# Optimization experiments

Hardware: AMD Instinct MI355X
Metric: run time of the kernel (lower is better)

The kernel has to match this reference:

```python
import jax, jax.numpy as jnp
import numpy as np

B, N, M, D = 256, 256, 256, 4
BIG = 1e10  # stand-in for +inf that keeps grads of unselected branches finite


def chamfer_split(target, reco, in_pid, out_pid):
    # masks of 'real' (non-zero pid) particles
    mask_x = in_pid != 0          # [B, N]
    mask_y = out_pid != 0         # [B, M]
    nx = jnp.sum(mask_x, axis=-1)  # [B] actual counts
    ny = jnp.sum(mask_y, axis=-1)
    n_in = jnp.maximum(1, nx).astype(target.dtype)   # max(1, n_in_part)
    n_out = jnp.maximum(1, ny).astype(target.dtype)  # max(1, n_out_part)

    # pairwise euclidean distances [B, N, M]
    diff = target[:, :, None, :] - reco[:, None, :, :]   # [B, N, M, D]
    dist = jnp.sqrt(jnp.sum(diff * diff, axis=-1))       # [B, N, M]

    # masked dual-axis mins (invalid entries pushed to BIG)
    min_xy = jnp.min(jnp.where(mask_y[:, None, :], dist, BIG), axis=-1)  # [B, N]
    min_yx = jnp.min(jnp.where(mask_x[:, :, None], dist, BIG), axis=-2)  # [B, M]
    sum_xy = jnp.sum(jnp.where(mask_x, min_xy, 0.0), axis=-1)  # [B]
    sum_yx = jnp.sum(jnp.where(mask_y, min_yx, 0.0), axis=-1)  # [B]

    normal = 0.5 * (sum_xy / n_out + sum_yx / n_in)  # [B]

    # edge cases: no reco non-zero particles -> sum||x_nz|| / max(1,nx);
    # no target non-zero particles -> sum over empty set = 0
    norm_x = jnp.linalg.norm(target, axis=-1)                    # [B, N]
    sum_norm_x_nz = jnp.sum(jnp.where(mask_x, norm_x, 0.0), -1)  # [B]
    eucl_non_zero = jnp.where(ny == 0, sum_norm_x_nz / n_in,
                              jnp.where(nx == 0, jnp.zeros_like(normal), normal))

    # zero-pid reco particles: mean L2 norm over zero entries
    norm_y = jnp.linalg.norm(reco, axis=-1)                          # [B, M]
    sum_norm_y_zero = jnp.sum(jnp.where(~mask_y, norm_y, 0.0), -1)   # [B]
    n_zero = jnp.maximum(1, reco.shape[1] - ny).astype(reco.dtype)
    eucl_zero = sum_norm_y_zero / n_zero

    # reduction == 'mean'
    return jnp.mean(eucl_non_zero), jnp.mean(eucl_zero)


def setup_inputs() -> dict:
    key = jax.random.key(0)
    k1, k2, k3, k4 = jax.random.split(key, 4)
    target = jax.random.normal(k1, (B, N, D), dtype=jnp.float32)
    reco = jax.random.normal(k2, (B, M, D), dtype=jnp.float32)
    in_pid = jax.random.randint(k3, (B, N), 0, 5, dtype=jnp.int32)
    out_pid = jax.random.randint(k4, (B, M), 0, 5, dtype=jnp.int32)
    return {"target": target, "reco": reco, "in_pid": in_pid, "out_pid": out_pid}


def reference(target, reco, in_pid, out_pid):
    return chamfer_split(target, reco, in_pid, out_pid)
```

## Files before the change

### kernel.cpp

```cpp
#include <hip/hip_runtime.h>
#include <math.h>

#define BB 256
#define NN 256
#define MM 256

#define POISON  1.0e18f
#define MINSENT 3.0e38f

__global__ __launch_bounds__(1024) void chamfer_batch_kernel(
    const float* __restrict__ target,
    const float* __restrict__ reco,
    const int*   __restrict__ in_pid,
    const int*   __restrict__ out_pid,
    float* __restrict__ out)
{
    const int b = blockIdx.x;
    const int t = threadIdx.x;

    __shared__ float4 sT[NN];
    __shared__ float4 sR[MM];
    __shared__ __align__(16) float sTh[NN];
    __shared__ __align__(16) float sRh[MM];
    __shared__ float sRn[MM];
    __shared__ int   sMx[NN], sMy[MM];
    __shared__ float pmin1[16][NN];
    __shared__ float pmin2[16][MM];
    __shared__ int   cnt[8];
    __shared__ float wred[8][2];

    if (t < 512) {
        const bool isT = (t < 256);
        const int  i   = isT ? t : (t - 256);
        const float4* src = isT ? (const float4*)(target + (size_t)b * NN * 4)
                                : (const float4*)(reco   + (size_t)b * MM * 4);
        const int*    pid = isT ? (in_pid + b * NN) : (out_pid + b * MM);
        float4 p = src[i];
        const int m = (pid[i] != 0);
        const float rawsq = fmaf(p.x, p.x, fmaf(p.y, p.y, fmaf(p.z, p.z, p.w * p.w)));
        float4 pp = m ? p : make_float4(POISON, POISON, POISON, POISON);
        const float ppsq = m ? rawsq : (4.0f * POISON * POISON);
        if (isT) {
            sT[i]  = pp;
            sTh[i] = ppsq;
            sMx[i] = m;
        } else {
            sR[i]  = pp;
            sRh[i] = ppsq;
            sMy[i] = m;
            sRn[i] = sqrtf(rawsq);
        }
        const unsigned long long bal = __ballot(m);
        if ((t & 63) == 0) cnt[t >> 6] = (int)__popcll(bal);
    }
    __syncthreads();

    {
        const bool pass1 = (t < 512);
        const int  u = pass1 ? t : (t - 512);
        const int  c = u >> 5;
        const int  g = u & 31;
        const float4* own    = pass1 ? sT : sR;
        const float4* other  = pass1 ? sR : sT;
        const float4* otherH = pass1 ? (const float4*)sRh : (const float4*)sTh;
        float (*pout)[256]   = pass1 ? pmin1 : pmin2;

        float4 n2[8];
        float  hx[8];
        #pragma unroll
        for (int k = 0; k < 8; ++k) {
            const float4 p = own[g + (k << 5)];
            n2[k] = make_float4(-2.f * p.x, -2.f * p.y, -2.f * p.z, -2.f * p.w);
            hx[k] = fmaf(p.x, p.x, fmaf(p.y, p.y, fmaf(p.z, p.z, p.w * p.w)));
        }
        float mn[8];
        #pragma unroll
        for (int k = 0; k < 8; ++k) mn[k] = MINSENT;

        const int base = c << 4;
        #pragma unroll
        for (int j = 0; j < 4; ++j) {
            const float4 hy4 = otherH[(c << 2) + j];
            #pragma unroll
            for (int i = 0; i < 4; ++i) {
                const float4 r  = other[base + (j << 2) + i];
                const float  hy = (i == 0) ? hy4.x : (i == 1) ? hy4.y : (i == 2) ? hy4.z : hy4.w;
                #pragma unroll
                for (int k = 0; k < 8; ++k) {
                    float acc = fmaf(n2[k].x, r.x, hx[k]);
                    acc = fmaf(n2[k].y, r.y, acc);
                    acc = fmaf(n2[k].z, r.z, acc);
                    acc = fmaf(n2[k].w, r.w, acc);
                    mn[k] = fminf(mn[k], acc + hy);
                }
            }
        }
        #pragma unroll
        for (int k = 0; k < 8; ++k) pout[c][g + (k << 5)] = mn[k];
    }
    __syncthreads();

    if (t < 512) {
        const bool rows = (t < 256);
        const int  i = rows ? t : (t - 256);
        float (*pm)[256] = rows ? pmin1 : pmin2;
        float m = pm[0][i];
        #pragma unroll
        for (int c = 1; c < 16; ++c) m = fminf(m, pm[c][i]);
        m = fmaxf(m, 0.0f);
        const int msk = rows ? sMx[i] : sMy[i];
        float va, vb;
        if (rows) {
            va = msk ? sqrtf(m) : 0.f;
            vb = msk ? sqrtf(sTh[i]) : 0.f;
        } else {
            va = msk ? sqrtf(m) : 0.f;
            vb = msk ? 0.f : sRn[i];
        }
        #pragma unroll
        for (int off = 32; off > 0; off >>= 1) {
            va += __shfl_down(va, off, 64);
            vb += __shfl_down(vb, off, 64);
        }
        if ((t & 63) == 0) {
            wred[t >> 6][0] = va;
            wred[t >> 6][1] = vb;
        }
    }
    __syncthreads();

    if (t == 0) {
        float s_xy = 0.f, s_nx = 0.f, s_yx = 0.f, s_ny0 = 0.f;
        int nx = 0, ny = 0;
        #pragma unroll
        for (int w = 0; w < 4; ++w) {
            s_xy  += wred[w][0];
            s_nx  += wred[w][1];
            s_yx  += wred[w + 4][0];
            s_ny0 += wred[w + 4][1];
            nx    += cnt[w];
            ny    += cnt[w + 4];
        }
        const float n_in  = (float)max(1, nx);
        const float n_out = (float)max(1, ny);
        const float normal = 0.5f * (s_xy / n_out + s_yx / n_in);
        const float eucl_nz = (ny == 0) ? (s_nx / n_in)
                                        : ((nx == 0) ? 0.0f : normal);
        const float n_zero = (float)max(1, MM - ny);
        const float eucl_z = s_ny0 / n_zero;
        atomicAdd(&out[0], eucl_nz * (1.0f / BB));
        atomicAdd(&out[1], eucl_z  * (1.0f / BB));
    }
}

extern "C" void kernel_launch(void* const* d_in, const int* in_sizes, int n_in,
                              void* d_out, int out_size, void* d_ws, size_t ws_size,
                              hipStream_t stream) {
    const float* target  = (const float*)d_in[0];
    const float* reco    = (const float*)d_in[1];
    const int*   in_pid  = (const int*)d_in[2];
    const int*   out_pid = (const int*)d_in[3];
    float* out = (float*)d_out;

    hipMemsetAsync(out, 0, (size_t)out_size * sizeof(float), stream);

    chamfer_batch_kernel<<<dim3(BB), dim3(1024), 0, stream>>>(
        target, reco, in_pid, out_pid, out);
}
```

Measured before the change: 72.84 us.

## Use packed f2 FMA with SoA shared layout and two-stage final reduction

Pairwise distance evaluation now uses 2-wide vector FMA/min so the compiler can emit packed fp32 instructions. The other point set is stored in structure-of-arrays shared buffers and read as float4 vectors. Work is split into 8 chunks of 32 columns instead of 16 chunks of 16, which halves the partial-min reduction. The per-batch atomicAdd plus memset is replaced by a per-batch workspace write and a tiny second reduction kernel, which adds a launch but removes the atomics and the memset.

```diff
diff --git a/kernel.cpp b/kernel.cpp
--- a/kernel.cpp
+++ b/kernel.cpp
@@ -7,25 +7,26 @@
 
 #define POISON  1.0e18f
 #define MINSENT 3.0e38f
+
+typedef float f2 __attribute__((ext_vector_type(2)));
+__device__ __forceinline__ f2 splat2(float v) { f2 r; r.x = v; r.y = v; return r; }
 
 __global__ __launch_bounds__(1024) void chamfer_batch_kernel(
     const float* __restrict__ target,
     const float* __restrict__ reco,
     const int*   __restrict__ in_pid,
     const int*   __restrict__ out_pid,
-    float* __restrict__ out)
+    float2* __restrict__ ws)
 {
     const int b = blockIdx.x;
     const int t = threadIdx.x;
 
-    __shared__ float4 sT[NN];
-    __shared__ float4 sR[MM];
-    __shared__ __align__(16) float sTh[NN];
-    __shared__ __align__(16) float sRh[MM];
+    __shared__ float4 sT[NN], sR[MM];
+    __shared__ __align__(16) float sTx[NN], sTy[NN], sTz[NN], sTw[NN], sTh[NN];
+    __shared__ __align__(16) float sRx[MM], sRy[MM], sRz[MM], sRw[MM], sRh[MM];
     __shared__ float sRn[MM];
     __shared__ int   sMx[NN], sMy[MM];
-    __shared__ float pmin1[16][NN];
-    __shared__ float pmin2[16][MM];
+    __shared__ float pmin1[8][NN], pmin2[8][MM];
     __shared__ int   cnt[8];
     __shared__ float wred[8][2];
 
@@ -41,12 +42,12 @@
         float4 pp = m ? p : make_float4(POISON, POISON, POISON, POISON);
         const float ppsq = m ? rawsq : (4.0f * POISON * POISON);
         if (isT) {
-            sT[i]  = pp;
-            sTh[i] = ppsq;
+            sT[i] = pp;
+            sTx[i] = pp.x; sTy[i] = pp.y; sTz[i] = pp.z; sTw[i] = pp.w; sTh[i] = ppsq;
             sMx[i] = m;
         } else {
-            sR[i]  = pp;
-            sRh[i] = ppsq;
+            sR[i] = pp;
+            sRx[i] = pp.x; sRy[i] = pp.y; sRz[i] = pp.z; sRw[i] = pp.w; sRh[i] = ppsq;
             sMy[i] = m;
             sRn[i] = sqrtf(rawsq);
         }
@@ -58,45 +59,63 @@
     {
         const bool pass1 = (t < 512);
         const int  u = pass1 ? t : (t - 512);
-        const int  c = u >> 5;
-        const int  g = u & 31;
-        const float4* own    = pass1 ? sT : sR;
-        const float4* other  = pass1 ? sR : sT;
-        const float4* otherH = pass1 ? (const float4*)sRh : (const float4*)sTh;
-        float (*pout)[256]   = pass1 ? pmin1 : pmin2;
-
-        float4 n2[8];
-        float  hx[8];
-        #pragma unroll
-        for (int k = 0; k < 8; ++k) {
-            const float4 p = own[g + (k << 5)];
-            n2[k] = make_float4(-2.f * p.x, -2.f * p.y, -2.f * p.z, -2.f * p.w);
-            hx[k] = fmaf(p.x, p.x, fmaf(p.y, p.y, fmaf(p.z, p.z, p.w * p.w)));
-        }
-        float mn[8];
-        #pragma unroll
-        for (int k = 0; k < 8; ++k) mn[k] = MINSENT;
-
-        const int base = c << 4;
-        #pragma unroll
-        for (int j = 0; j < 4; ++j) {
-            const float4 hy4 = otherH[(c << 2) + j];
+        const int  c = u >> 6;
+        const int  g = u & 63;
+        const float4* own  = pass1 ? sT  : sR;
+        const float*  ownH = pass1 ? sTh : sRh;
+        const float*  ox   = pass1 ? sRx : sTx;
+        const float*  oy   = pass1 ? sRy : sTy;
+        const float*  oz   = pass1 ? sRz : sTz;
+        const float*  owp  = pass1 ? sRw : sTw;
+        const float*  oh   = pass1 ? sRh : sTh;
+        float (*pout)[256] = pass1 ? pmin1 : pmin2;
+
+        f2 n2x[4], n2y[4], n2z[4], n2w[4], hx[4], mn[4];
+        #pragma unroll
+        for (int k = 0; k < 4; ++k) {
+            const float4 p = own[g + (k << 6)];
+            n2x[k] = splat2(-2.f * p.x);
+            n2y[k] = splat2(-2.f * p.y);
+            n2z[k] = splat2(-2.f * p.z);
+            n2w[k] = splat2(-2.f * p.w);
+            hx[k]  = splat2(ownH[g + (k << 6)]);
+            mn[k]  = splat2(MINSENT);
+        }
+
+        const int base = c << 5;
+        #pragma unroll
+        for (int q = 0; q < 8; ++q) {
+            const int o = base + (q << 2);
+            const float4 rx4 = *(const float4*)&ox[o];
+            const float4 ry4 = *(const float4*)&oy[o];
+            const float4 rz4 = *(const float4*)&oz[o];
+            const float4 rw4 = *(const float4*)&owp[o];
+            const float4 rh4 = *(const float4*)&oh[o];
+            f2 rx0, rx1, ry0, ry1, rz0, rz1, rw0, rw1, rh0, rh1;
+            rx0.x = rx4.x; rx0.y = rx4.y;  rx1.x = rx4.z; rx1.y = rx4.w;
+            ry0.x = ry4.x; ry0.y = ry4.y;  ry1.x = ry4.z; ry1.y = ry4.w;
+            rz0.x = rz4.x; rz0.y = rz4.y;  rz1.x = rz4.z; rz1.y = rz4.w;
+            rw0.x = rw4.x; rw0.y = rw4.y;  rw1.x = rw4.z; rw1.y = rw4.w;
+            rh0.x = rh4.x; rh0.y = rh4.y;  rh1.x = rh4.z; rh1.y = rh4.w;
             #pragma unroll
-            for (int i = 0; i < 4; ++i) {
-                const float4 r  = other[base + (j << 2) + i];
-                const float  hy = (i == 0) ? hy4.x : (i == 1) ? hy4.y : (i == 2) ? hy4.z : hy4.w;
-                #pragma unroll
-                for (int k = 0; k < 8; ++k) {
-                    float acc = fmaf(n2[k].x, r.x, hx[k]);
-                    acc = fmaf(n2[k].y, r.y, acc);
-                    acc = fmaf(n2[k].z, r.z, acc);
-                    acc = fmaf(n2[k].w, r.w, acc);
-                    mn[k] = fminf(mn[k], acc + hy);
-                }
+            for (int k = 0; k < 4; ++k) {
+                f2 a0 = __builtin_elementwise_fma(n2x[k], rx0, hx[k]);
+                a0 = __builtin_elementwise_fma(n2y[k], ry0, a0);
+                a0 = __builtin_elementwise_fma(n2z[k], rz0, a0);
+                a0 = __builtin_elementwise_fma(n2w[k], rw0, a0);
+                a0 = a0 + rh0;
+                mn[k] = __builtin_elementwise_min(mn[k], a0);
+                f2 a1 = __builtin_elementwise_fma(n2x[k], rx1, hx[k]);
+                a1 = __builtin_elementwise_fma(n2y[k], ry1, a1);
+                a1 = __builtin_elementwise_fma(n2z[k], rz1, a1);
+                a1 = __builtin_elementwise_fma(n2w[k], rw1, a1);
+                a1 = a1 + rh1;
+                mn[k] = __builtin_elementwise_min(mn[k], a1);
             }
         }
         #pragma unroll
-        for (int k = 0; k < 8; ++k) pout[c][g + (k << 5)] = mn[k];
+        for (int k = 0; k < 4; ++k)
+            pout[c][g + (k << 6)] = fminf(mn[k].x, mn[k].y);
     }
     __syncthreads();
 
@@ -106,7 +125,7 @@
         float (*pm)[256] = rows ? pmin1 : pmin2;
         float m = pm[0][i];
         #pragma unroll
-        for (int c = 1; c < 16; ++c) m = fminf(m, pm[c][i]);
+        for (int c2 = 1; c2 < 8; ++c2) m = fminf(m, pm[c2][i]);
         m = fmaxf(m, 0.0f);
         const int msk = rows ? sMx[i] : sMy[i];
         float va, vb;
@@ -148,8 +167,29 @@
                                         : ((nx == 0) ? 0.0f : normal);
         const float n_zero = (float)max(1, MM - ny);
         const float eucl_z = s_ny0 / n_zero;
-        atomicAdd(&out[0], eucl_nz * (1.0f / BB));
-        atomicAdd(&out[1], eucl_z  * (1.0f / BB));
+        ws[b] = make_float2(eucl_nz, eucl_z);
+    }
+}
+
+__global__ __launch_bounds__(64) void chamfer_final_kernel(
+    const float2* __restrict__ ws, float* __restrict__ out)
+{
+    const int t = threadIdx.x;
+    float a = 0.f, z = 0.f;
+    #pragma unroll
+    for (int k = 0; k < 4; ++k) {
+        const float2 v = ws[t + (k << 6)];
+        a += v.x;
+        z += v.y;
+    }
+    #pragma unroll
+    for (int off = 32; off > 0; off >>= 1) {
+        a += __shfl_down(a, off, 64);
+        z += __shfl_down(z, off, 64);
+    }
+    if (t == 0) {
+        out[0] = a * (1.0f / BB);
+        out[1] = z * (1.0f / BB);
     }
 }
 
@@ -161,9 +201,9 @@
     const int*   in_pid  = (const int*)d_in[2];
     const int*   out_pid = (const int*)d_in[3];
     float* out = (float*)d_out;
-
-    hipMemsetAsync(out, 0, (size_t)out_size * sizeof(float), stream);
+    float2* ws = (float2*)d_ws;
 
     chamfer_batch_kernel<<<dim3(BB), dim3(1024), 0, stream>>>(
-        target, reco, in_pid, out_pid, out);
+        target, reco, in_pid, out_pid, ws);
+    chamfer_final_kernel<<<dim3(1), dim3(64), 0, stream>>>(ws, out);
 }
```

Measured after the change: 66.65 us (median of 2 runs). 8.5% less time.
